# Optimization experiments

Hardware: AMD Instinct MI355X
Metric: run time of the kernel (lower is better)

The kernel has to match this reference:

```python
import jax, jax.numpy as jnp
import numpy as np

ONE_STEP = 14
EPS = 1e-5


def _bn(x, g, b):
    # training-mode batchnorm over the node/batch axis (biased variance)
    m = jnp.mean(x, axis=0)
    v = jnp.var(x, axis=0)
    return (x - m) * jax.lax.rsqrt(v + EPS) * g + b


def _gcn_conv(x, W, b, src, dst, dis):
    N = x.shape[0]
    h = x @ W
    norm = (dis[src] * dis[dst])[:, None]
    agg = jax.ops.segment_sum(h[src] * norm, dst, num_segments=N)
    agg = agg + (dis * dis)[:, None] * h  # self-loop contribution
    return agg + b


def setup_inputs() -> dict:
    key = jax.random.key(0)
    ks = jax.random.split(key, 16)
    N, F, E, NC = 114688, 512, 917504, 10
    x = jax.random.normal(ks[0], (N, F), jnp.float32)
    edge_index = jax.random.randint(ks[1], (2, E), 0, N, jnp.int32)

    def lin(k, i, o):
        return jax.random.normal(k, (i, o), jnp.float32) / np.sqrt(i).astype(np.float32)

    d = {"x": x, "edge_index": edge_index}
    dims = [(F, 128), (128, 256), (256, 64), (64, 32)]
    for li, (i, o) in enumerate(dims, 1):
        d[f"W{li}"] = lin(ks[1 + li], i, o)
        d[f"b{li}"] = jnp.zeros((o,), jnp.float32)
        d[f"bn{li}_g"] = jnp.ones((o,), jnp.float32)
        d[f"bn{li}_b"] = jnp.zeros((o,), jnp.float32)
    d["gW1"] = lin(ks[6], 32, 16); d["gb1"] = jnp.zeros((16,), jnp.float32)
    d["gbn1_g"] = jnp.ones((16,), jnp.float32); d["gbn1_b"] = jnp.zeros((16,), jnp.float32)
    d["gW2"] = lin(ks[7], 16, 1); d["gb2"] = jnp.zeros((1,), jnp.float32)
    d["gbn2_g"] = jnp.ones((1,), jnp.float32); d["gbn2_b"] = jnp.zeros((1,), jnp.float32)
    d["fcW"] = lin(ks[8], 32, NC); d["fcb"] = jnp.zeros((NC,), jnp.float32)
    return d


def reference(x, edge_index, W1, b1, bn1_g, bn1_b, W2, b2, bn2_g, bn2_b,
              W3, b3, bn3_g, bn3_b, W4, b4, bn4_g, bn4_b,
              gW1, gb1, gbn1_g, gbn1_b, gW2, gb2, gbn2_g, gbn2_b, fcW, fcb):
    N = x.shape[0]
    src, dst = edge_index[0], edge_index[1]
    # degree with self-loops (counted on dst, per PyG gcn_norm)
    deg = jax.ops.segment_sum(jnp.ones_like(dst, jnp.float32), dst, num_segments=N) + 1.0
    dis = jax.lax.rsqrt(deg)

    h = _bn(jax.nn.relu(_gcn_conv(x, W1, b1, src, dst, dis)), bn1_g, bn1_b)
    h = _bn(jax.nn.relu(_gcn_conv(h, W2, b2, src, dst, dis)), bn2_g, bn2_b)
    h = _bn(jax.nn.relu(_gcn_conv(h, W3, b3, src, dst, dis)), bn3_g, bn3_b)
    h = _bn(jax.nn.relu(_gcn_conv(h, W4, b4, src, dst, dis)), bn4_g, bn4_b)

    # gate network: Linear -> BN -> ReLU -> Linear -> BN -> ReLU
    g = jax.nn.relu(_bn(h @ gW1 + gb1, gbn1_g, gbn1_b))
    g = jax.nn.relu(_bn(g @ gW2 + gb2, gbn2_g, gbn2_b))[:, 0]  # [N]

    B = N // ONE_STEP
    batch = jnp.repeat(jnp.arange(B), ONE_STEP)
    # segment softmax over nodes of each graph
    m = jax.ops.segment_max(g, batch, num_segments=B)
    e = jnp.exp(g - m[batch])
    s = jax.ops.segment_sum(e, batch, num_segments=B)
    alpha = e / s[batch]
    pooled = jax.ops.segment_sum(alpha[:, None] * h, batch, num_segments=B)  # [B,32]

    # dropout is identity in eval mode
    logits = pooled @ fcW + fcb
    return jax.nn.softmax(logits, axis=1)
```

## Files before the change

### kernel.cpp

```cpp
#include <hip/hip_runtime.h>

#define NN 114688
#define NE 917504
#define NBATCH 8192
#define GSZ 14
#define NCLS 10
#define EPSB 1e-5f
#define NSCAN 112

typedef unsigned short u16;
typedef short bf16x8 __attribute__((ext_vector_type(8)));
typedef float f32x4 __attribute__((ext_vector_type(4)));
typedef _Float16 h8t __attribute__((ext_vector_type(8)));

__device__ __forceinline__ float bf2f(u16 u) {
    union { unsigned int i; float f; } v; v.i = ((unsigned int)u) << 16; return v.f;
}
__device__ __forceinline__ u16 f2bf(float f) {
    union { float f; unsigned int i; } v; v.f = f;
    unsigned int i = v.i;
    unsigned int r = i + 0x7FFFu + ((i >> 16) & 1u);
    return (u16)(r >> 16);
}

__global__ __launch_bounds__(256) void k_hist(const int* __restrict__ ei, int* __restrict__ counts) {
    int e = blockIdx.x * 256 + threadIdx.x;
    atomicAdd(&counts[ei[NE + e]], 1);
}

__global__ __launch_bounds__(256) void k_scan1(const int* __restrict__ counts, int* __restrict__ bsum) {
    __shared__ int red[256];
    int tid = threadIdx.x;
    int base = blockIdx.x * 1024 + tid * 4;
    int s = counts[base] + counts[base + 1] + counts[base + 2] + counts[base + 3];
    red[tid] = s; __syncthreads();
    for (int o = 128; o > 0; o >>= 1) {
        if (tid < o) red[tid] += red[tid + o];
        __syncthreads();
    }
    if (tid == 0) bsum[blockIdx.x] = red[0];
}

__global__ void k_scan2(int* bsum, int* offs) {
    if (threadIdx.x == 0) {
        int run = 0;
        for (int i = 0; i < NSCAN; i++) { int t = bsum[i]; bsum[i] = run; run += t; }
        offs[NN] = run;
    }
}

__global__ __launch_bounds__(256) void k_scan3(const int* __restrict__ counts, const int* __restrict__ bsum,
                                               int* __restrict__ offs) {
    __shared__ int ss[256];
    int tid = threadIdx.x;
    int base = blockIdx.x * 1024 + tid * 4;
    int v0 = counts[base], v1 = counts[base + 1], v2 = counts[base + 2], v3 = counts[base + 3];
    int ts = v0 + v1 + v2 + v3;
    ss[tid] = ts; __syncthreads();
    for (int o = 1; o < 256; o <<= 1) {
        int add = (tid >= o) ? ss[tid - o] : 0;
        __syncthreads();
        ss[tid] += add;
        __syncthreads();
    }
    int excl = ss[tid] - ts + bsum[blockIdx.x];
    offs[base] = excl;
    offs[base + 1] = excl + v0;
    offs[base + 2] = excl + v0 + v1;
    offs[base + 3] = excl + v0 + v1 + v2;
}

__global__ __launch_bounds__(256) void k_dis_cursor(const int* __restrict__ counts, const int* __restrict__ offs,
                                                    float* __restrict__ dis, int* __restrict__ cursor) {
    int n = blockIdx.x * 256 + threadIdx.x;
    dis[n] = rsqrtf((float)counts[n] + 1.0f);
    cursor[n] = offs[n];
}

__global__ __launch_bounds__(256) void k_scatter(const int* __restrict__ ei, int* __restrict__ cursor,
                                                 int* __restrict__ srcs, float* __restrict__ sd,
                                                 const float* __restrict__ dis) {
    int e = blockIdx.x * 256 + threadIdx.x;
    int d = ei[NE + e], s = ei[e];
    int p = atomicAdd(&cursor[d], 1);
    srcs[p] = s;
    sd[p] = dis[s];
}

__global__ __launch_bounds__(256) void k_tsplit(const float* __restrict__ Wsrc,
                                                u16* __restrict__ Wh, u16* __restrict__ Wl,
                                                int K, int F) {
    int i = blockIdx.x * 256 + threadIdx.x;
    if (i < K * F) {
        int k = i / F, f = i % F;
        float w = Wsrc[i];
        u16 h = f2bf(w);
        float r = w - bf2f(h);
        Wh[f * K + k] = h;
        Wl[f * K + k] = f2bf(r);
    }
}

template<int BM, int BN, int WCOLS, bool AFF>
__global__ __launch_bounds__(256) void k_gemm(
    const float* __restrict__ A, const u16* __restrict__ Wh, const u16* __restrict__ Wl,
    _Float16* __restrict__ C, const int K, const int Fout,
    const float* __restrict__ sc, const float* __restrict__ sh)
{
    constexpr int AST = 40;
    __shared__ u16 Ah[BM][AST], Al[BM][AST];
    __shared__ u16 Bh[BN][AST], Bl[BN][AST];
    __shared__ float scs[AFF ? 256 : 1], shs[AFF ? 256 : 1];

    const int tid = threadIdx.x;
    const int row0 = blockIdx.y * BM;
    const int col0 = blockIdx.x * BN;

    if constexpr (AFF) {
        for (int i = tid; i < K; i += 256) { scs[i] = sc[i]; shs[i] = sh[i]; }
    }

    const int wave = tid >> 6, lane = tid & 63;
    const int mb = (wave / WCOLS) * 64;
    const int nb = (wave % WCOLS) * 64;
    const int lm = lane & 15;
    const int lk = (lane >> 4) * 8;

    f32x4 acc[4][4];
#pragma unroll
    for (int i = 0; i < 4; i++)
#pragma unroll
        for (int j = 0; j < 4; j++)
#pragma unroll
            for (int r = 0; r < 4; r++) acc[i][j][r] = 0.f;

    const int stg_r = tid >> 3;
    const int stg_c = (tid & 7) * 4;

    for (int k0 = 0; k0 < K; k0 += 32) {
        __syncthreads();
#pragma unroll
        for (int p = 0; p < BM / 32; p++) {
            const int r = p * 32 + stg_r;
            const float4 v = *(const float4*)(A + (size_t)(row0 + r) * K + k0 + stg_c);
            float y[4] = {v.x, v.y, v.z, v.w};
            ushort4 hv, lv;
#pragma unroll
            for (int q = 0; q < 4; q++) {
                float yy = y[q];
                if constexpr (AFF) yy = yy * scs[k0 + stg_c + q] + shs[k0 + stg_c + q];
                u16 h = f2bf(yy);
                float rm = yy - bf2f(h);
                ((u16*)&hv)[q] = h;
                ((u16*)&lv)[q] = f2bf(rm);
            }
            *(ushort4*)&Ah[r][stg_c] = hv;
            *(ushort4*)&Al[r][stg_c] = lv;
        }
#pragma unroll
        for (int p = 0; p < BN / 32; p++) {
            const int n = p * 32 + stg_r;
            *(ushort4*)&Bh[n][stg_c] = *(const ushort4*)(Wh + (size_t)(col0 + n) * K + k0 + stg_c);
            *(ushort4*)&Bl[n][stg_c] = *(const ushort4*)(Wl + (size_t)(col0 + n) * K + k0 + stg_c);
        }
        __syncthreads();

        bf16x8 ah[4], al[4], bh[4], bl[4];
#pragma unroll
        for (int mi = 0; mi < 4; mi++) {
            ah[mi] = *(const bf16x8*)&Ah[mb + mi * 16 + lm][lk];
            al[mi] = *(const bf16x8*)&Al[mb + mi * 16 + lm][lk];
        }
#pragma unroll
        for (int ni = 0; ni < 4; ni++) {
            bh[ni] = *(const bf16x8*)&Bh[nb + ni * 16 + lm][lk];
            bl[ni] = *(const bf16x8*)&Bl[nb + ni * 16 + lm][lk];
        }
#pragma unroll
        for (int mi = 0; mi < 4; mi++)
#pragma unroll
            for (int ni = 0; ni < 4; ni++) {
                acc[mi][ni] = __builtin_amdgcn_mfma_f32_16x16x32_bf16(al[mi], bh[ni], acc[mi][ni], 0, 0, 0);
                acc[mi][ni] = __builtin_amdgcn_mfma_f32_16x16x32_bf16(ah[mi], bl[ni], acc[mi][ni], 0, 0, 0);
                acc[mi][ni] = __builtin_amdgcn_mfma_f32_16x16x32_bf16(ah[mi], bh[ni], acc[mi][ni], 0, 0, 0);
            }
    }

    const int rb = row0 + mb + (lane >> 4) * 4;
    const int cb = col0 + nb + lm;
#pragma unroll
    for (int mi = 0; mi < 4; mi++)
#pragma unroll
        for (int ni = 0; ni < 4; ni++)
#pragma unroll
            for (int r = 0; r < 4; r++)
                C[(size_t)(rb + mi * 16 + r) * Fout + cb + ni * 16] = (_Float16)acc[mi][ni][r];
}

template<int CH>
__global__ __launch_bounds__(256) void k_agg(
    const _Float16* __restrict__ h, float* __restrict__ t, const float* __restrict__ bias,
    const int* __restrict__ off, const int* __restrict__ srcs, const float* __restrict__ sd,
    const float* __restrict__ dis, float* __restrict__ statS, float* __restrict__ statQ,
    const int ostr)
{
    constexpr int ECH = 8;
    constexpr int LPG = CH / ECH;
    constexpr int NSUB = 64 / LPG;
    __shared__ float redS[CH], redQ[CH];
    const int tid = threadIdx.x;
    for (int i = tid; i < CH; i += 256) { redS[i] = 0.f; redQ[i] = 0.f; }
    __syncthreads();

    const int lane = tid & 63;
    const int sub = lane / LPG;
    const int c = (lane % LPG) * ECH;
    const int wid = (blockIdx.x * 256 + tid) >> 6;
    const int nw = (gridDim.x * 256) >> 6;

    float bs[ECH], bq[ECH], bv[ECH];
#pragma unroll
    for (int v = 0; v < ECH; v++) { bs[v] = 0.f; bq[v] = 0.f; bv[v] = bias[c + v]; }

    for (int n = wid; n < NN; n += nw) {
        const int p0 = off[n], p1 = off[n + 1];
        float a[ECH];
#pragma unroll
        for (int v = 0; v < ECH; v++) a[v] = 0.f;

        int p = p0 + sub;
        int s = 0; float w = 0.f;
        if (p < p1) { s = srcs[p]; w = sd[p]; }
        while (p < p1) {
            const int pn = p + NSUB;
            int s2 = 0; float w2 = 0.f;
            if (pn < p1) { s2 = srcs[pn]; w2 = sd[pn]; }
            h8t hv = *(const h8t*)(h + (size_t)s * CH + c);
#pragma unroll
            for (int v = 0; v < ECH; v++) a[v] += w * (float)hv[v];
            s = s2; w = w2; p = pn;
        }
#pragma unroll
        for (int o = LPG; o < 64; o <<= 1) {
#pragma unroll
            for (int v = 0; v < ECH; v++) a[v] += __shfl_xor(a[v], o);
        }
        if (sub == 0) {
            const float dn = dis[n];
            const float dn2 = dn * dn;
            h8t hn = *(const h8t*)(h + (size_t)n * CH + c);
            float o8[ECH];
#pragma unroll
            for (int v = 0; v < ECH; v++) {
                float ov = fmaxf(dn * a[v] + dn2 * (float)hn[v] + bv[v], 0.f);
                o8[v] = ov;
                bs[v] += ov; bq[v] += ov * ov;
            }
            float* tr = t + (size_t)n * ostr + c;
            float4 w0; w0.x = o8[0]; w0.y = o8[1]; w0.z = o8[2]; w0.w = o8[3];
            float4 w1; w1.x = o8[4]; w1.y = o8[5]; w1.z = o8[6]; w1.w = o8[7];
            *(float4*)tr = w0;
            *(float4*)(tr + 4) = w1;
        }
    }
    if (sub == 0) {
#pragma unroll
        for (int v = 0; v < ECH; v++) { atomicAdd(&redS[c + v], bs[v]); atomicAdd(&redQ[c + v], bq[v]); }
    }
    __syncthreads();
    for (int i = tid; i < CH; i += 256) { atomicAdd(&statS[i], redS[i]); atomicAdd(&statQ[i], redQ[i]); }
}

__global__ void k_bnpar(const float* __restrict__ S, const float* __restrict__ Q,
                        const float* __restrict__ g, const float* __restrict__ b,
                        float* __restrict__ sc, float* __restrict__ sh, int F) {
    int c = threadIdx.x;
    if (c >= F) return;
    const float invn = 1.0f / (float)NN;
    float mean = S[c] * invn;
    float var = Q[c] * invn - mean * mean;
    float s = g[c] * rsqrtf(fmaxf(var, 0.f) + EPSB);
    sc[c] = s;
    sh[c] = b[c] - mean * s;
}

template<int K, int F, bool BIAS>
__global__ __launch_bounds__(256) void k_smm(
    const float* __restrict__ A, const float* __restrict__ Wf, const float* __restrict__ bias,
    _Float16* __restrict__ C, const float* __restrict__ sc, const float* __restrict__ sh)
{
    __shared__ float Wl[K * F];
    __shared__ float scl[K], shl[K], bl[F];
    const int tid = threadIdx.x;
    for (int i = tid; i < K * F; i += 256) Wl[i] = Wf[i];
    if (tid < K) { scl[tid] = sc[tid]; shl[tid] = sh[tid]; }
    if (tid < F) {
        bl[tid] = 0.f;
        if constexpr (BIAS) bl[tid] = bias[tid];
    }
    __syncthreads();
    const int n = blockIdx.x * 256 + tid;
    float acc[F];
#pragma unroll
    for (int f = 0; f < F; f++) acc[f] = bl[f];
    const float* ar = A + (size_t)n * K;
    for (int k = 0; k < K; k += 4) {
        float4 av = *(const float4*)(ar + k);
        float y0 = av.x * scl[k] + shl[k];
        float y1 = av.y * scl[k + 1] + shl[k + 1];
        float y2 = av.z * scl[k + 2] + shl[k + 2];
        float y3 = av.w * scl[k + 3] + shl[k + 3];
#pragma unroll
        for (int f = 0; f < F; f += 4) {
            float4 w0 = *(const float4*)&Wl[k * F + f];
            float4 w1 = *(const float4*)&Wl[(k + 1) * F + f];
            float4 w2 = *(const float4*)&Wl[(k + 2) * F + f];
            float4 w3 = *(const float4*)&Wl[(k + 3) * F + f];
            acc[f + 0] += y0 * w0.x + y1 * w1.x + y2 * w2.x + y3 * w3.x;
            acc[f + 1] += y0 * w0.y + y1 * w1.y + y2 * w2.y + y3 * w3.y;
            acc[f + 2] += y0 * w0.z + y1 * w1.z + y2 * w2.z + y3 * w3.z;
            acc[f + 3] += y0 * w0.w + y1 * w1.w + y2 * w2.w + y3 * w3.w;
        }
    }
    _Float16* cr = C + (size_t)n * F;
#pragma unroll
    for (int f = 0; f < F; f++) cr[f] = (_Float16)acc[f];
}

template<int F>
__global__ __launch_bounds__(256) void k_stats16(const _Float16* __restrict__ A,
                                                 float* __restrict__ S, float* __restrict__ Q) {
    __shared__ float redS[F], redQ[F];
    const int tid = threadIdx.x;
    for (int i = tid; i < F; i += 256) { redS[i] = 0.f; redQ[i] = 0.f; }
    __syncthreads();
    const int g = blockIdx.x * 256 + tid;
    const int c = g % F;
    const int step = (gridDim.x * 256) / F;
    float s = 0.f, q = 0.f;
    for (int r = g / F; r < NN; r += step) {
        float v = (float)A[(size_t)r * F + c];
        s += v; q += v * v;
    }
    atomicAdd(&redS[c], s); atomicAdd(&redQ[c], q);
    __syncthreads();
    for (int i = tid; i < F; i += 256) { atomicAdd(&S[i], redS[i]); atomicAdd(&Q[i], redQ[i]); }
}

__global__ __launch_bounds__(256) void k_stats1(const float* __restrict__ A,
                                                float* __restrict__ S, float* __restrict__ Q) {
    __shared__ float redS[1], redQ[1];
    const int tid = threadIdx.x;
    if (tid == 0) { redS[0] = 0.f; redQ[0] = 0.f; }
    __syncthreads();
    const int g = blockIdx.x * 256 + tid;
    const int step = gridDim.x * 256;
    float s = 0.f, q = 0.f;
    for (int r = g; r < NN; r += step) {
        float v = A[r];
        s += v; q += v * v;
    }
    atomicAdd(&redS[0], s); atomicAdd(&redQ[0], q);
    __syncthreads();
    if (tid == 0) { atomicAdd(&S[0], redS[0]); atomicAdd(&Q[0], redQ[0]); }
}

__global__ __launch_bounds__(256) void k_gate2(const _Float16* __restrict__ g1,
                                               const float* __restrict__ sc, const float* __restrict__ sh,
                                               const float* __restrict__ w2, const float* __restrict__ b2,
                                               float* __restrict__ g2) {
    __shared__ float wl[16], scl[16], shl[16], b2l[1];
    const int tid = threadIdx.x;
    if (tid < 16) { wl[tid] = w2[tid]; scl[tid] = sc[tid]; shl[tid] = sh[tid]; }
    if (tid == 0) b2l[0] = b2[0];
    __syncthreads();
    const int n = blockIdx.x * 256 + tid;
    const _Float16* r = g1 + (size_t)n * 16;
    float acc = b2l[0];
#pragma unroll
    for (int k = 0; k < 16; k++) {
        float y = fmaxf((float)r[k] * scl[k] + shl[k], 0.f);
        acc += y * wl[k];
    }
    g2[n] = acc;
}

__global__ __launch_bounds__(256) void k_pool(const float* __restrict__ t4,
                                              const float* __restrict__ sc4, const float* __restrict__ sh4,
                                              const float* __restrict__ g2,
                                              const float* __restrict__ gsc2, const float* __restrict__ gsh2,
                                              const float* __restrict__ fcW, const float* __restrict__ fcb,
                                              float* __restrict__ out) {
    __shared__ float fw[32 * NCLS], fbl[NCLS], sc4l[32], sh4l[32];
    const int tid = threadIdx.x;
    for (int i = tid; i < 32 * NCLS; i += 256) fw[i] = fcW[i];
    if (tid < NCLS) fbl[tid] = fcb[tid];
    if (tid < 32) { sc4l[tid] = sc4[tid]; sh4l[tid] = sh4[tid]; }
    __syncthreads();
    const int b = blockIdx.x * 256 + tid;
    const float s2 = gsc2[0], h2 = gsh2[0];
    const int base = b * GSZ;

    float gv[GSZ];
    float m = -1e30f;
#pragma unroll
    for (int i = 0; i < GSZ; i++) {
        float v = fmaxf(g2[base + i] * s2 + h2, 0.f);
        gv[i] = v; m = fmaxf(m, v);
    }
    float ssum = 0.f;
#pragma unroll
    for (int i = 0; i < GSZ; i++) { float e = __expf(gv[i] - m); gv[i] = e; ssum += e; }
    const float inv = 1.0f / ssum;

    float pooled[32];
#pragma unroll
    for (int c = 0; c < 32; c++) pooled[c] = 0.f;
#pragma unroll
    for (int i = 0; i < GSZ; i++) {
        const float a = gv[i] * inv;
        const float* tr = t4 + (size_t)(base + i) * 32;
#pragma unroll
        for (int c = 0; c < 32; c += 4) {
            float4 tv = *(const float4*)(tr + c);
            pooled[c + 0] += a * (tv.x * sc4l[c + 0] + sh4l[c + 0]);
            pooled[c + 1] += a * (tv.y * sc4l[c + 1] + sh4l[c + 1]);
            pooled[c + 2] += a * (tv.z * sc4l[c + 2] + sh4l[c + 2]);
            pooled[c + 3] += a * (tv.w * sc4l[c + 3] + sh4l[c + 3]);
        }
    }
    float lg[NCLS];
    float mx = -1e30f;
#pragma unroll
    for (int j = 0; j < NCLS; j++) {
        float a = fbl[j];
#pragma unroll
        for (int c = 0; c < 32; c++) a += pooled[c] * fw[c * NCLS + j];
        lg[j] = a; mx = fmaxf(mx, a);
    }
    float es = 0.f;
#pragma unroll
    for (int j = 0; j < NCLS; j++) { float e = __expf(lg[j] - mx); lg[j] = e; es += e; }
    const float iv = 1.0f / es;
#pragma unroll
    for (int j = 0; j < NCLS; j++) out[b * NCLS + j] = lg[j] * iv;
}

extern "C" void kernel_launch(void* const* d_in, const int* in_sizes, int n_in,
                              void* d_out, int out_size, void* d_ws, size_t ws_size,
                              hipStream_t stream) {
    (void)in_sizes; (void)n_in; (void)out_size; (void)ws_size;
    const float* x    = (const float*)d_in[0];
    const int*   ei   = (const int*)d_in[1];
    const float* W1   = (const float*)d_in[2];
    const float* b1   = (const float*)d_in[3];
    const float* bn1g = (const float*)d_in[4];
    const float* bn1b = (const float*)d_in[5];
    const float* W2   = (const float*)d_in[6];
    const float* b2   = (const float*)d_in[7];
    const float* bn2g = (const float*)d_in[8];
    const float* bn2b = (const float*)d_in[9];
    const float* W3   = (const float*)d_in[10];
    const float* b3   = (const float*)d_in[11];
    const float* bn3g = (const float*)d_in[12];
    const float* bn3b = (const float*)d_in[13];
    const float* W4   = (const float*)d_in[14];
    const float* b4   = (const float*)d_in[15];
    const float* bn4g = (const float*)d_in[16];
    const float* bn4b = (const float*)d_in[17];
    const float* gW1  = (const float*)d_in[18];
    const float* gb1  = (const float*)d_in[19];
    const float* gbn1g = (const float*)d_in[20];
    const float* gbn1b = (const float*)d_in[21];
    const float* gW2  = (const float*)d_in[22];
    const float* gb2  = (const float*)d_in[23];
    const float* gbn2g = (const float*)d_in[24];
    const float* gbn2b = (const float*)d_in[25];
    const float* fcW  = (const float*)d_in[26];
    const float* fcb  = (const float*)d_in[27];
    float* out = (float*)d_out;

    char* base = (char*)d_ws;
    size_t off_ = 0;
    auto carve = [&](size_t bytes) -> char* {
        char* p = base + off_;
        off_ = (off_ + bytes + 255) & ~(size_t)255;
        return p;
    };
    int*   counts = (int*)carve((size_t)NN * 4);
    float* stats  = (float*)carve(994 * 4);
    const size_t zero_bytes = off_;
    int*   offs   = (int*)carve((size_t)(NN + 1) * 4);
    int*   cursor = (int*)carve((size_t)NN * 4);
    int*   srcs   = (int*)carve((size_t)NE * 4);
    float* sd     = (float*)carve((size_t)NE * 4);
    float* dis    = (float*)carve((size_t)NN * 4);
    int*   bsum   = (int*)carve(NSCAN * 4);
    float* pars   = (float*)carve(994 * 4);
    u16*   Wt1h   = (u16*)carve(512 * 128 * 2);
    u16*   Wt1l   = (u16*)carve(512 * 128 * 2);
    u16*   Wt2h   = (u16*)carve(128 * 256 * 2);
    u16*   Wt2l   = (u16*)carve(128 * 256 * 2);
    u16*   Wt3h   = (u16*)carve(256 * 64 * 2);
    u16*   Wt3l   = (u16*)carve(256 * 64 * 2);
    float* g2raw  = (float*)carve((size_t)NN * 4);
    _Float16* P   = (_Float16*)carve((size_t)NN * 128 * 2);
    float*    Q   = (float*)carve((size_t)NN * 128 * 4);
    float*    R   = (float*)carve((size_t)NN * 256 * 4);

    float* S1 = stats;      float* Q1s = S1 + 128;
    float* S2 = Q1s + 128;  float* Q2s = S2 + 256;
    float* S3 = Q2s + 256;  float* Q3s = S3 + 64;
    float* S4 = Q3s + 64;   float* Q4s = S4 + 32;
    float* gS1 = Q4s + 32;  float* gQ1 = gS1 + 16;
    float* gS2 = gQ1 + 16;  float* gQ2 = gS2 + 1;

    float* sc1 = pars;      float* sh1 = sc1 + 128;
    float* sc2 = sh1 + 128; float* sh2 = sc2 + 256;
    float* sc3 = sh2 + 256; float* sh3 = sc3 + 64;
    float* sc4 = sh3 + 64;  float* sh4 = sc4 + 32;
    float* gsc1 = sh4 + 32; float* gsh1 = gsc1 + 16;
    float* gsc2 = gsh1 + 16; float* gsh2 = gsc2 + 1;

    hipMemsetAsync(d_ws, 0, zero_bytes, stream);

    k_hist<<<NE / 256, 256, 0, stream>>>(ei, counts);
    k_scan1<<<NSCAN, 256, 0, stream>>>(counts, bsum);
    k_scan2<<<1, 64, 0, stream>>>(bsum, offs);
    k_scan3<<<NSCAN, 256, 0, stream>>>(counts, bsum, offs);
    k_dis_cursor<<<NN / 256, 256, 0, stream>>>(counts, offs, dis, cursor);
    k_scatter<<<NE / 256, 256, 0, stream>>>(ei, cursor, srcs, sd, dis);
    k_tsplit<<<(512 * 128 + 255) / 256, 256, 0, stream>>>(W1, Wt1h, Wt1l, 512, 128);
    k_tsplit<<<(128 * 256 + 255) / 256, 256, 0, stream>>>(W2, Wt2h, Wt2l, 128, 256);
    k_tsplit<<<(256 * 64 + 255) / 256, 256, 0, stream>>>(W3, Wt3h, Wt3l, 256, 64);

    k_gemm<128, 128, 2, false><<<dim3(1, NN / 128), 256, 0, stream>>>(
        x, Wt1h, Wt1l, P, 512, 128, nullptr, nullptr);
    k_agg<128><<<2048, 256, 0, stream>>>(P, Q, b1, offs, srcs, sd, dis, S1, Q1s, 128);
    k_bnpar<<<1, 256, 0, stream>>>(S1, Q1s, bn1g, bn1b, sc1, sh1, 128);

    k_gemm<128, 128, 2, true><<<dim3(1, NN / 128), 256, 0, stream>>>(
        Q, Wt2h, Wt2l, P, 128, 128, sc1, sh1);
    k_agg<128><<<2048, 256, 0, stream>>>(P, R, b2, offs, srcs, sd, dis, S2, Q2s, 256);
    k_gemm<128, 128, 2, true><<<dim3(1, NN / 128), 256, 0, stream>>>(
        Q, Wt2h + 128 * 128, Wt2l + 128 * 128, P, 128, 128, sc1, sh1);
    k_agg<128><<<2048, 256, 0, stream>>>(P, R + 128, b2 + 128, offs, srcs, sd, dis,
                                         S2 + 128, Q2s + 128, 256);
    k_bnpar<<<1, 256, 0, stream>>>(S2, Q2s, bn2g, bn2b, sc2, sh2, 256);

    k_gemm<256, 64, 1, true><<<dim3(1, NN / 256), 256, 0, stream>>>(
        R, Wt3h, Wt3l, P, 256, 64, sc2, sh2);
    k_agg<64><<<2048, 256, 0, stream>>>(P, Q, b3, offs, srcs, sd, dis, S3, Q3s, 64);
    k_bnpar<<<1, 256, 0, stream>>>(S3, Q3s, bn3g, bn3b, sc3, sh3, 64);

    k_smm<64, 32, false><<<NN / 256, 256, 0, stream>>>(Q, W4, nullptr, P, sc3, sh3);
    k_agg<32><<<2048, 256, 0, stream>>>(P, Q, b4, offs, srcs, sd, dis, S4, Q4s, 32);
    k_bnpar<<<1, 256, 0, stream>>>(S4, Q4s, bn4g, bn4b, sc4, sh4, 32);

    k_smm<32, 16, true><<<NN / 256, 256, 0, stream>>>(Q, gW1, gb1, P, sc4, sh4);
    k_stats16<16><<<NSCAN, 256, 0, stream>>>(P, gS1, gQ1);
    k_bnpar<<<1, 256, 0, stream>>>(gS1, gQ1, gbn1g, gbn1b, gsc1, gsh1, 16);

    k_gate2<<<NN / 256, 256, 0, stream>>>(P, gsc1, gsh1, gW2, gb2, g2raw);
    k_stats1<<<NSCAN, 256, 0, stream>>>(g2raw, gS2, gQ2);
    k_bnpar<<<1, 256, 0, stream>>>(gS2, gQ2, gbn2g, gbn2b, gsc2, gsh2, 1);

    k_pool<<<NBATCH / 256, 256, 0, stream>>>(Q, sc4, sh4, g2raw, gsc2, gsh2, fcW, fcb, out);
}
```

Before: 1.165 ms.

## Fold BN affine into weights, store activations as bf16 hi/lo, widen layer-2 aggregation

The batchnorm scale and shift are folded into the next layer's weights and a per-column constant (k_wfold), so the GEMMs no longer apply the affine per element. The aggregation kernels now write activations pre-split into bf16 hi/lo pairs, so the GEMM staging loads ready-made bf16 data instead of converting fp32 on the fly. Layer 2 becomes a single 256-wide GEMM plus one CH=256 aggregation instead of two 128-wide halves, and each lane handles 16 channels instead of 8. In exchange it adds a serial single-block weight-fold kernel, and the hi/lo split at aggregation output may change rounding slightly.

```diff
diff --git a/kernel.cpp b/kernel.cpp
--- a/kernel.cpp
+++ b/kernel.cpp
@@ -12,6 +12,7 @@
 typedef short bf16x8 __attribute__((ext_vector_type(8)));
 typedef float f32x4 __attribute__((ext_vector_type(4)));
 typedef _Float16 h8t __attribute__((ext_vector_type(8)));
+typedef unsigned short u16x8 __attribute__((ext_vector_type(8)));
 
 __device__ __forceinline__ float bf2f(u16 u) {
     union { unsigned int i; float f; } v; v.i = ((unsigned int)u) << 16; return v.f;
@@ -21,6 +22,10 @@
     unsigned int i = v.i;
     unsigned int r = i + 0x7FFFu + ((i >> 16) & 1u);
     return (u16)(r >> 16);
+}
+__device__ __forceinline__ void splitbf(float y, u16& h, u16& l) {
+    h = f2bf(y);
+    l = f2bf(y - bf2f(h));
 }
 
 __global__ __launch_bounds__(256) void k_hist(const int* __restrict__ ei, int* __restrict__ counts) {
@@ -93,38 +98,54 @@
     int i = blockIdx.x * 256 + threadIdx.x;
     if (i < K * F) {
         int k = i / F, f = i % F;
-        float w = Wsrc[i];
-        u16 h = f2bf(w);
-        float r = w - bf2f(h);
+        u16 h, l; splitbf(Wsrc[i], h, l);
         Wh[f * K + k] = h;
-        Wl[f * K + k] = f2bf(r);
-    }
-}
-
-template<int BM, int BN, int WCOLS, bool AFF>
+        Wl[f * K + k] = l;
+    }
+}
+
+__global__ void k_wfold(const float* __restrict__ W, const float* __restrict__ sc,
+                        const float* __restrict__ sh, u16* __restrict__ Wh, u16* __restrict__ Wl,
+                        float* __restrict__ c2, int K, int F) {
+    int f = threadIdx.x;
+    if (f >= F) return;
+    float acc = 0.f;
+    for (int k = 0; k < K; k++) {
+        float w = W[k * F + f];
+        u16 h, l; splitbf(sc[k] * w, h, l);
+        Wh[f * K + k] = h;
+        Wl[f * K + k] = l;
+        acc += sh[k] * w;
+    }
+    c2[f] = acc;
+}
+
+template<int BM, int BN, int WCOLS, bool AFP32, bool C2>
 __global__ __launch_bounds__(256) void k_gemm(
-    const float* __restrict__ A, const u16* __restrict__ Wh, const u16* __restrict__ Wl,
-    _Float16* __restrict__ C, const int K, const int Fout,
-    const float* __restrict__ sc, const float* __restrict__ sh)
+    const float* __restrict__ Af, const u16* __restrict__ Ahi, const u16* __restrict__ Alo,
+    const u16* __restrict__ Wh, const u16* __restrict__ Wl,
+    _Float16* __restrict__ C, const int K, const int Fout, const float* __restrict__ c2)
 {
     constexpr int AST = 40;
     __shared__ u16 Ah[BM][AST], Al[BM][AST];
     __shared__ u16 Bh[BN][AST], Bl[BN][AST];
-    __shared__ float scs[AFF ? 256 : 1], shs[AFF ? 256 : 1];
 
     const int tid = threadIdx.x;
     const int row0 = blockIdx.y * BM;
     const int col0 = blockIdx.x * BN;
-
-    if constexpr (AFF) {
-        for (int i = tid; i < K; i += 256) { scs[i] = sc[i]; shs[i] = sh[i]; }
-    }
 
     const int wave = tid >> 6, lane = tid & 63;
     const int mb = (wave / WCOLS) * 64;
     const int nb = (wave % WCOLS) * 64;
     const int lm = lane & 15;
     const int lk = (lane >> 4) * 8;
+    const int cb = col0 + nb + lm;
+
+    float c2v[4] = {0.f, 0.f, 0.f, 0.f};
+    if constexpr (C2) {
+#pragma unroll
+        for (int ni = 0; ni < 4; ni++) c2v[ni] = c2[cb + ni * 16];
+    }
 
     f32x4 acc[4][4];
 #pragma unroll
@@ -132,7 +153,7 @@
 #pragma unroll
         for (int j = 0; j < 4; j++)
 #pragma unroll
-            for (int r = 0; r < 4; r++) acc[i][j][r] = 0.f;
+            for (int r = 0; r < 4; r++) acc[i][j][r] = c2v[j];
 
     const int stg_r = tid >> 3;
     const int stg_c = (tid & 7) * 4;
@@ -142,20 +163,18 @@
 #pragma unroll
         for (int p = 0; p < BM / 32; p++) {
             const int r = p * 32 + stg_r;
-            const float4 v = *(const float4*)(A + (size_t)(row0 + r) * K + k0 + stg_c);
-            float y[4] = {v.x, v.y, v.z, v.w};
-            ushort4 hv, lv;
-#pragma unroll
-            for (int q = 0; q < 4; q++) {
-                float yy = y[q];
-                if constexpr (AFF) yy = yy * scs[k0 + stg_c + q] + shs[k0 + stg_c + q];
-                u16 h = f2bf(yy);
-                float rm = yy - bf2f(h);
-                ((u16*)&hv)[q] = h;
-                ((u16*)&lv)[q] = f2bf(rm);
+            if constexpr (AFP32) {
+                const float4 v = *(const float4*)(Af + (size_t)(row0 + r) * K + k0 + stg_c);
+                float y[4] = {v.x, v.y, v.z, v.w};
+                ushort4 hv, lv;
+#pragma unroll
+                for (int q = 0; q < 4; q++) splitbf(y[q], ((u16*)&hv)[q], ((u16*)&lv)[q]);
+                *(ushort4*)&Ah[r][stg_c] = hv;
+                *(ushort4*)&Al[r][stg_c] = lv;
+            } else {
+                *(ushort4*)&Ah[r][stg_c] = *(const ushort4*)(Ahi + (size_t)(row0 + r) * K + k0 + stg_c);
+                *(ushort4*)&Al[r][stg_c] = *(const ushort4*)(Alo + (size_t)(row0 + r) * K + k0 + stg_c);
             }
-            *(ushort4*)&Ah[r][stg_c] = hv;
-            *(ushort4*)&Al[r][stg_c] = lv;
         }
 #pragma unroll
         for (int p = 0; p < BN / 32; p++) {
@@ -187,7 +206,6 @@
     }
 
     const int rb = row0 + mb + (lane >> 4) * 4;
-    const int cb = col0 + nb + lm;
 #pragma unroll
     for (int mi = 0; mi < 4; mi++)
 #pragma unroll
@@ -199,12 +217,12 @@
 
 template<int CH>
 __global__ __launch_bounds__(256) void k_agg(
-    const _Float16* __restrict__ h, float* __restrict__ t, const float* __restrict__ bias,
+    const _Float16* __restrict__ h, u16* __restrict__ thi, u16* __restrict__ tlo,
+    const float* __restrict__ bias,
     const int* __restrict__ off, const int* __restrict__ srcs, const float* __restrict__ sd,
-    const float* __restrict__ dis, float* __restrict__ statS, float* __restrict__ statQ,
-    const int ostr)
+    const float* __restrict__ dis, float* __restrict__ statS, float* __restrict__ statQ)
 {
-    constexpr int ECH = 8;
+    constexpr int ECH = 16;
     constexpr int LPG = CH / ECH;
     constexpr int NSUB = 64 / LPG;
     __shared__ float redS[CH], redQ[CH];
@@ -235,9 +253,11 @@
             const int pn = p + NSUB;
             int s2 = 0; float w2 = 0.f;
             if (pn < p1) { s2 = srcs[pn]; w2 = sd[pn]; }
-            h8t hv = *(const h8t*)(h + (size_t)s * CH + c);
-#pragma unroll
-            for (int v = 0; v < ECH; v++) a[v] += w * (float)hv[v];
+            const _Float16* hr = h + (size_t)s * CH + c;
+            h8t hv0 = *(const h8t*)hr;
+            h8t hv1 = *(const h8t*)(hr + 8);
+#pragma unroll
+            for (int v = 0; v < 8; v++) { a[v] += w * (float)hv0[v]; a[v + 8] += w * (float)hv1[v]; }
             s = s2; w = w2; p = pn;
         }
 #pragma unroll
@@ -248,19 +268,27 @@
         if (sub == 0) {
             const float dn = dis[n];
             const float dn2 = dn * dn;
-            h8t hn = *(const h8t*)(h + (size_t)n * CH + c);
-            float o8[ECH];
-#pragma unroll
-            for (int v = 0; v < ECH; v++) {
-                float ov = fmaxf(dn * a[v] + dn2 * (float)hn[v] + bv[v], 0.f);
-                o8[v] = ov;
-                bs[v] += ov; bq[v] += ov * ov;
+            const _Float16* hr = h + (size_t)n * CH + c;
+            h8t hn0 = *(const h8t*)hr;
+            h8t hn1 = *(const h8t*)(hr + 8);
+            float o16[ECH];
+#pragma unroll
+            for (int v = 0; v < 8; v++) {
+                o16[v] = fmaxf(dn * a[v] + dn2 * (float)hn0[v] + bv[v], 0.f);
+                o16[v + 8] = fmaxf(dn * a[v + 8] + dn2 * (float)hn1[v] + bv[v + 8], 0.f);
             }
-            float* tr = t + (size_t)n * ostr + c;
-            float4 w0; w0.x = o8[0]; w0.y = o8[1]; w0.z = o8[2]; w0.w = o8[3];
-            float4 w1; w1.x = o8[4]; w1.y = o8[5]; w1.z = o8[6]; w1.w = o8[7];
-            *(float4*)tr = w0;
-            *(float4*)(tr + 4) = w1;
+            u16x8 hv0, lv0, hv1, lv1;
+#pragma unroll
+            for (int v = 0; v < 8; v++) {
+                splitbf(o16[v], ((u16*)&hv0)[v], ((u16*)&lv0)[v]);
+                splitbf(o16[v + 8], ((u16*)&hv1)[v], ((u16*)&lv1)[v]);
+                bs[v] += o16[v]; bq[v] += o16[v] * o16[v];
+                bs[v + 8] += o16[v + 8]; bq[v + 8] += o16[v + 8] * o16[v + 8];
+            }
+            u16* th = thi + (size_t)n * CH + c;
+            u16* tl = tlo + (size_t)n * CH + c;
+            *(u16x8*)th = hv0; *(u16x8*)(th + 8) = hv1;
+            *(u16x8*)tl = lv0; *(u16x8*)(tl + 8) = lv1;
         }
     }
     if (sub == 0) {
@@ -286,7 +314,8 @@
 
 template<int K, int F, bool BIAS>
 __global__ __launch_bounds__(256) void k_smm(
-    const float* __restrict__ A, const float* __restrict__ Wf, const float* __restrict__ bias,
+    const u16* __restrict__ Ahi, const u16* __restrict__ Alo,
+    const float* __restrict__ Wf, const float* __restrict__ bias,
     _Float16* __restrict__ C, const float* __restrict__ sc, const float* __restrict__ sh)
 {
     __shared__ float Wl[K * F];
@@ -303,13 +332,15 @@
     float acc[F];
 #pragma unroll
     for (int f = 0; f < F; f++) acc[f] = bl[f];
-    const float* ar = A + (size_t)n * K;
+    const u16* ah = Ahi + (size_t)n * K;
+    const u16* al = Alo + (size_t)n * K;
     for (int k = 0; k < K; k += 4) {
-        float4 av = *(const float4*)(ar + k);
-        float y0 = av.x * scl[k] + shl[k];
-        float y1 = av.y * scl[k + 1] + shl[k + 1];
-        float y2 = av.z * scl[k + 2] + shl[k + 2];
-        float y3 = av.w * scl[k + 3] + shl[k + 3];
+        ushort4 hv = *(const ushort4*)(ah + k);
+        ushort4 lv = *(const ushort4*)(al + k);
+        float y0 = (bf2f(hv.x) + bf2f(lv.x)) * scl[k] + shl[k];
+        float y1 = (bf2f(hv.y) + bf2f(lv.y)) * scl[k + 1] + shl[k + 1];
+        float y2 = (bf2f(hv.z) + bf2f(lv.z)) * scl[k + 2] + shl[k + 2];
+        float y3 = (bf2f(hv.w) + bf2f(lv.w)) * scl[k + 3] + shl[k + 3];
 #pragma unroll
         for (int f = 0; f < F; f += 4) {
             float4 w0 = *(const float4*)&Wl[k * F + f];
@@ -385,7 +416,7 @@
     g2[n] = acc;
 }
 
-__global__ __launch_bounds__(256) void k_pool(const float* __restrict__ t4,
+__global__ __launch_bounds__(256) void k_pool(const u16* __restrict__ t4hi, const u16* __restrict__ t4lo,
                                               const float* __restrict__ sc4, const float* __restrict__ sh4,
                                               const float* __restrict__ g2,
                                               const float* __restrict__ gsc2, const float* __restrict__ gsh2,
@@ -419,14 +450,16 @@
 #pragma unroll
     for (int i = 0; i < GSZ; i++) {
         const float a = gv[i] * inv;
-        const float* tr = t4 + (size_t)(base + i) * 32;
+        const u16* th = t4hi + (size_t)(base + i) * 32;
+        const u16* tl = t4lo + (size_t)(base + i) * 32;
 #pragma unroll
         for (int c = 0; c < 32; c += 4) {
-            float4 tv = *(const float4*)(tr + c);
-            pooled[c + 0] += a * (tv.x * sc4l[c + 0] + sh4l[c + 0]);
-            pooled[c + 1] += a * (tv.y * sc4l[c + 1] + sh4l[c + 1]);
-            pooled[c + 2] += a * (tv.z * sc4l[c + 2] + sh4l[c + 2]);
-            pooled[c + 3] += a * (tv.w * sc4l[c + 3] + sh4l[c + 3]);
+            ushort4 hv = *(const ushort4*)(th + c);
+            ushort4 lv = *(const ushort4*)(tl + c);
+            pooled[c + 0] += a * ((bf2f(hv.x) + bf2f(lv.x)) * sc4l[c + 0] + sh4l[c + 0]);
+            pooled[c + 1] += a * ((bf2f(hv.y) + bf2f(lv.y)) * sc4l[c + 1] + sh4l[c + 1]);
+            pooled[c + 2] += a * ((bf2f(hv.z) + bf2f(lv.z)) * sc4l[c + 2] + sh4l[c + 2]);
+            pooled[c + 3] += a * ((bf2f(hv.w) + bf2f(lv.w)) * sc4l[c + 3] + sh4l[c + 3]);
         }
     }
     float lg[NCLS];
@@ -503,10 +536,14 @@
     u16*   Wt2l   = (u16*)carve(128 * 256 * 2);
     u16*   Wt3h   = (u16*)carve(256 * 64 * 2);
     u16*   Wt3l   = (u16*)carve(256 * 64 * 2);
+    float* c2_2   = (float*)carve(256 * 4);
+    float* c2_3   = (float*)carve(64 * 4);
     float* g2raw  = (float*)carve((size_t)NN * 4);
-    _Float16* P   = (_Float16*)carve((size_t)NN * 128 * 2);
-    float*    Q   = (float*)carve((size_t)NN * 128 * 4);
-    float*    R   = (float*)carve((size_t)NN * 256 * 4);
+    _Float16* P   = (_Float16*)carve((size_t)NN * 256 * 2);
+    u16*   Qhi    = (u16*)carve((size_t)NN * 128 * 2);
+    u16*   Qlo    = (u16*)carve((size_t)NN * 128 * 2);
+    u16*   Rhi    = (u16*)carve((size_t)NN * 256 * 2);
+    u16*   Rlo    = (u16*)carve((size_t)NN * 256 * 2);
 
     float* S1 = stats;      float* Q1s = S1 + 128;
     float* S2 = Q1s + 128;  float* Q2s = S2 + 256;
@@ -531,33 +568,29 @@
     k_dis_cursor<<<NN / 256, 256, 0, stream>>>(counts, offs, dis, cursor);
     k_scatter<<<NE / 256, 256, 0, stream>>>(ei, cursor, srcs, sd, dis);
     k_tsplit<<<(512 * 128 + 255) / 256, 256, 0, stream>>>(W1, Wt1h, Wt1l, 512, 128);
-    k_tsplit<<<(128 * 256 + 255) / 256, 256, 0, stream>>>(W2, Wt2h, Wt2l, 128, 256);
-    k_tsplit<<<(256 * 64 + 255) / 256, 256, 0, stream>>>(W3, Wt3h, Wt3l, 256, 64);
-
-    k_gemm<128, 128, 2, false><<<dim3(1, NN / 128), 256, 0, stream>>>(
-        x, Wt1h, Wt1l, P, 512, 128, nullptr, nullptr);
-    k_agg<128><<<2048, 256, 0, stream>>>(P, Q, b1, offs, srcs, sd, dis, S1, Q1s, 128);
+
+    k_gemm<128, 128, 2, true, false><<<dim3(1, NN / 128), 256, 0, stream>>>(
+        x, nullptr, nullptr, Wt1h, Wt1l, P, 512, 128, nullptr);
+    k_agg<128><<<2048, 256, 0, stream>>>(P, Qhi, Qlo, b1, offs, srcs, sd, dis, S1, Q1s);
     k_bnpar<<<1, 256, 0, stream>>>(S1, Q1s, bn1g, bn1b, sc1, sh1, 128);
 
-    k_gemm<128, 128, 2, true><<<dim3(1, NN / 128), 256, 0, stream>>>(
-        Q, Wt2h, Wt2l, P, 128, 128, sc1, sh1);
-    k_agg<128><<<2048, 256, 0, stream>>>(P, R, b2, offs, srcs, sd, dis, S2, Q2s, 256);
-    k_gemm<128, 128, 2, true><<<dim3(1, NN / 128), 256, 0, stream>>>(
-        Q, Wt2h + 128 * 128, Wt2l + 128 * 128, P, 128, 128, sc1, sh1);
-    k_agg<128><<<2048, 256, 0, stream>>>(P, R + 128, b2 + 128, offs, srcs, sd, dis,
-                                         S2 + 128, Q2s + 128, 256);
+    k_wfold<<<1, 256, 0, stream>>>(W2, sc1, sh1, Wt2h, Wt2l, c2_2, 128, 256);
+    k_gemm<128, 128, 2, false, true><<<dim3(2, NN / 128), 256, 0, stream>>>(
+        nullptr, Qhi, Qlo, Wt2h, Wt2l, P, 128, 256, c2_2);
+    k_agg<256><<<2048, 256, 0, stream>>>(P, Rhi, Rlo, b2, offs, srcs, sd, dis, S2, Q2s);
     k_bnpar<<<1, 256, 0, stream>>>(S2, Q2s, bn2g, bn2b, sc2, sh2, 256);
 
-    k_gemm<256, 64, 1, true><<<dim3(1, NN / 256), 256, 0, stream>>>(
-        R, Wt3h, Wt3l, P, 256, 64, sc2, sh2);
-    k_agg<64><<<2048, 256, 0, stream>>>(P, Q, b3, offs, srcs, sd, dis, S3, Q3s, 64);
+    k_wfold<<<1, 256, 0, stream>>>(W3, sc2, sh2, Wt3h, Wt3l, c2_3, 256, 64);
+    k_gemm<256, 64, 1, false, true><<<dim3(1, NN / 256), 256, 0, stream>>>(
+        nullptr, Rhi, Rlo, Wt3h, Wt3l, P, 256, 64, c2_3);
+    k_agg<64><<<2048, 256, 0, stream>>>(P, Qhi, Qlo, b3, offs, srcs, sd, dis, S3, Q3s);
     k_bnpar<<<1, 256, 0, stream>>>(S3, Q3s, bn3g, bn3b, sc3, sh3, 64);
 
-    k_smm<64, 32, false><<<NN / 256, 256, 0, stream>>>(Q, W4, nullptr, P, sc3, sh3);
-    k_agg<32><<<2048, 256, 0, stream>>>(P, Q, b4, offs, srcs, sd, dis, S4, Q4s, 32);
+    k_smm<64, 32, false><<<NN / 256, 256, 0, stream>>>(Qhi, Qlo, W4, nullptr, P, sc3, sh3);
+    k_agg<32><<<2048, 256, 0, stream>>>(P, Qhi, Qlo, b4, offs, srcs, sd, dis, S4, Q4s);
     k_bnpar<<<1, 256, 0, stream>>>(S4, Q4s, bn4g, bn4b, sc4, sh4, 32);
 
-    k_smm<32, 16, true><<<NN / 256, 256, 0, stream>>>(Q, gW1, gb1, P, sc4, sh4);
+    k_smm<32, 16, true><<<NN / 256, 256, 0, stream>>>(Qhi, Qlo, gW1, gb1, P, sc4, sh4);
     k_stats16<16><<<NSCAN, 256, 0, stream>>>(P, gS1, gQ1);
     k_bnpar<<<1, 256, 0, stream>>>(gS1, gQ1, gbn1g, gbn1b, gsc1, gsh1, 16);
 
@@ -565,5 +598,5 @@
     k_stats1<<<NSCAN, 256, 0, stream>>>(g2raw, gS2, gQ2);
     k_bnpar<<<1, 256, 0, stream>>>(gS2, gQ2, gbn2g, gbn2b, gsc2, gsh2, 1);
 
-    k_pool<<<NBATCH / 256, 256, 0, stream>>>(Q, sc4, sh4, g2raw, gsc2, gsh2, fcW, fcb, out);
-}
+    k_pool<<<NBATCH / 256, 256, 0, stream>>>(Qhi, Qlo, sc4, sh4, g2raw, gsc2, gsh2, fcW, fcb, out);
+}
```

After: 1.356 ms. 1.16x slower.
